# Optimization experiments

Hardware: AMD Instinct MI355X
Metric: run time of the kernel (lower is better)

Reference implementation:

```python
import jax, jax.numpy as jnp
import numpy as np

HEADS = 4
C = 128            # per-head out channels (hard-coded 128 in the module)
NEG_SLOPE_ATT = 0.2   # GATConv attention leaky_relu slope
NEG_SLOPE = 0.01      # F.leaky_relu default slope


def _diag_output_ids(num_groups, n):
    # ids = base_i + n*j + j for group i, agent j; base_i = i * n^2
    i = np.arange(num_groups)[:, None] * (n * n)
    j = np.arange(n)[None, :] * (n + 1)
    return jnp.asarray((i + j).reshape(-1))


def setup_inputs() -> dict:
    key = jax.random.key(0)
    ks = jax.random.split(key, 12)
    num_groups, n_agents = 12, 48
    N = num_groups * n_agents * n_agents      # 27648 nodes
    E = 442368
    F_in, edge_dim, hidden = 256, 16, 256
    s = 0.05
    return {
        "x": jax.random.normal(ks[0], (N, F_in), jnp.float32),
        "edge_index": jax.random.randint(ks[1], (2, E), 0, N, jnp.int32),
        "edge_attr": jax.random.normal(ks[2], (E, edge_dim), jnp.float32),
        "num_groups": num_groups,
        "agents_per_group": n_agents,
        "W": jax.random.normal(ks[3], (F_in, HEADS * C), jnp.float32) * s,
        "att_src": jax.random.normal(ks[4], (HEADS, C), jnp.float32) * s,
        "att_dst": jax.random.normal(ks[5], (HEADS, C), jnp.float32) * s,
        "W_edge": jax.random.normal(ks[6], (edge_dim, HEADS * C), jnp.float32) * s,
        "att_edge": jax.random.normal(ks[7], (HEADS, C), jnp.float32) * s,
        "bias_gat": jnp.zeros((HEADS * C,), jnp.float32),
        "fc_W": jax.random.normal(ks[8], (HEADS * C, hidden), jnp.float32) * s,
        "fc_b": jnp.zeros((hidden,), jnp.float32),
    }


def _gat_conv(x, src, dst, edge_attr_full, W, att_src, att_dst, W_edge, att_edge, bias):
    N = x.shape[0]
    h = (x @ W).reshape(N, HEADS, C)                       # [N,H,C]
    a_src = jnp.einsum('nhc,hc->nh', h, att_src)           # [N,H]
    a_dst = jnp.einsum('nhc,hc->nh', h, att_dst)
    he = (edge_attr_full @ W_edge).reshape(-1, HEADS, C)   # [E',H,C]
    a_edge = jnp.einsum('ehc,hc->eh', he, att_edge)
    logits = jax.nn.leaky_relu(a_src[src] + a_dst[dst] + a_edge, NEG_SLOPE_ATT)
    # segment softmax over incoming edges of each dst node
    m = jax.ops.segment_max(logits, dst, num_segments=N)   # [N,H]
    e = jnp.exp(logits - m[dst])
    s = jax.ops.segment_sum(e, dst, num_segments=N)
    alpha = e / (s[dst] + 1e-16)                           # [E',H]
    msg = h[src] * alpha[..., None]                        # [E',H,C]
    out = jax.ops.segment_sum(msg, dst, num_segments=N)    # [N,H,C]
    return out.reshape(N, HEADS * C) + bias


def reference(x, edge_index, edge_attr, num_groups, agents_per_group,
              W, att_src, att_dst, W_edge, att_edge, bias_gat, fc_W, fc_b):
    N = x.shape[0]
    # add self-loops (PyG default), self-loop edge_attr = mean fill
    loops = jnp.arange(N, dtype=edge_index.dtype)
    src = jnp.concatenate([edge_index[0], loops])
    dst = jnp.concatenate([edge_index[1], loops])
    ea = jnp.concatenate([edge_attr,
                          jnp.broadcast_to(edge_attr.mean(0), (N, edge_attr.shape[1]))])
    h = jax.nn.leaky_relu(
        _gat_conv(x, src, dst, ea, W, att_src, att_dst, W_edge, att_edge, bias_gat),
        NEG_SLOPE)
    ids = _diag_output_ids(num_groups, agents_per_group)
    # fc_output + leaky_relu then diagonal index-select (select first: same math)
    return jax.nn.leaky_relu(h[ids] @ fc_W + fc_b, NEG_SLOPE)
```

## Files before the change

kernel.cpp:

```cpp
#include <hip/hip_runtime.h>

#define NNODES 27648
#define NEDGES 442368
#define FIN    256
#define HC     512
#define NH     4
#define CDIM   128
#define NAG    48
#define NGRP   12
#define N2     2304
#define NOUT   576
#define CAP    128
#define EDIM   16
#define MPART  512
#define SCANB  (NEDGES/256)
#define ASRCB0 (SCANB + 1)


__device__ __forceinline__ float lrelu(float v, float s){ return v > 0.0f ? v : s * v; }

__device__ __forceinline__ float wsum(float v){
  #pragma unroll
  for (int off = 32; off; off >>= 1) v += __shfl_xor(v, off, 64);
  return v;
}
__device__ __forceinline__ float wmax(float v){
  #pragma unroll
  for (int off = 32; off; off >>= 1) v = fmaxf(v, __shfl_xor(v, off, 64));
  return v;
}

__global__ __launch_bounds__(256) void k_pre(
    const float* __restrict__ W, const float* __restrict__ att_src,
    const float* __restrict__ att_dst, const float* __restrict__ W_edge,
    const float* __restrict__ att_edge, const float* __restrict__ ea,
    float* __restrict__ ws_, float* __restrict__ wd_, float* __restrict__ we_,
    int* __restrict__ counts, float4* __restrict__ easum_part){
  int b = blockIdx.x;
  int tid = threadIdx.x;
  if (b < 11) {
    int g = b * 256 + tid;
    if (g < 1024) {
      int f = g >> 2, h = g & 3;
      const float4* wp = (const float4*)(W + f*HC + h*CDIM);
      const float4* ap = (const float4*)(att_src + h*CDIM);
      float s = 0.f;
      #pragma unroll 8
      for (int c4 = 0; c4 < CDIM/4; c4++){
        float4 wv = wp[c4], av = ap[c4];
        s += wv.x*av.x + wv.y*av.y + wv.z*av.z + wv.w*av.w;
      }
      ws_[g] = s;
    } else if (g < 2048) {
      int gg = g - 1024; int f = gg >> 2, h = gg & 3;
      const float4* wp = (const float4*)(W + f*HC + h*CDIM);
      const float4* ap = (const float4*)(att_dst + h*CDIM);
      float s = 0.f;
      #pragma unroll 8
      for (int c4 = 0; c4 < CDIM/4; c4++){
        float4 wv = wp[c4], av = ap[c4];
        s += wv.x*av.x + wv.y*av.y + wv.z*av.z + wv.w*av.w;
      }
      wd_[gg] = s;
    } else if (g < 2112) {
      int gg = g - 2048; int d = gg >> 2, h = gg & 3;
      const float4* wp = (const float4*)(W_edge + d*HC + h*CDIM);
      const float4* ap = (const float4*)(att_edge + h*CDIM);
      float s = 0.f;
      #pragma unroll 8
      for (int c4 = 0; c4 < CDIM/4; c4++){
        float4 wv = wp[c4], av = ap[c4];
        s += wv.x*av.x + wv.y*av.y + wv.z*av.z + wv.w*av.w;
      }
      we_[gg] = s;
    } else if (g < 2112 + NOUT) {
      counts[g - 2112] = 0;
    }
  } else {
    int pb = b - 11;
    const float4* p = (const float4*)ea;
    const int total = NEDGES * 4;
    float4 acc = make_float4(0.f, 0.f, 0.f, 0.f);
    for (int i = pb*256 + tid; i < total; i += MPART*256){
      float4 v = p[i];
      acc.x += v.x; acc.y += v.y; acc.z += v.z; acc.w += v.w;
    }
    #pragma unroll
    for (int off = 4; off <= 32; off <<= 1){
      acc.x += __shfl_xor(acc.x, off, 64);
      acc.y += __shfl_xor(acc.y, off, 64);
      acc.z += __shfl_xor(acc.z, off, 64);
      acc.w += __shfl_xor(acc.w, off, 64);
    }
    __shared__ float4 sd4[16];
    int lane = tid & 63, wave = tid >> 6;
    if (lane < 4) sd4[wave*4 + lane] = acc;
    __syncthreads();
    if (tid < 4){
      float4 t = sd4[tid];
      float4 a = sd4[4+tid], c = sd4[8+tid], d = sd4[12+tid];
      t.x += a.x + c.x + d.x; t.y += a.y + c.y + d.y;
      t.z += a.z + c.z + d.z; t.w += a.w + c.w + d.w;
      easum_part[pb*4 + tid] = t;
    }
  }
}

__global__ __launch_bounds__(256) void k_scan(const int* __restrict__ ei,
    const float* __restrict__ ea, const float* __restrict__ we_,
    const float* __restrict__ ws_, const float* __restrict__ wd_,
    const float* __restrict__ x,
    int* __restrict__ counts, int* __restrict__ slist, float* __restrict__ aed,
    const float* __restrict__ easum_part, float* __restrict__ easum,
    float* __restrict__ mal, float* __restrict__ asrc, float* __restrict__ adst){
  int tid = threadIdx.x;
  int b = blockIdx.x;
  if (b < SCANB){
    int e = b*256 + tid;
    int dst = ei[NEDGES + e];
    int r = dst % N2;
    if (r % 49) return;
    int row = (dst / N2) * NAG + r / 49;
    int pos = atomicAdd(&counts[row], 1);
    if (pos >= CAP) return;
    slist[row*CAP + pos] = ei[e];
    const float* eap = ea + (size_t)e*EDIM;
    float a0=0.f,a1=0.f,a2=0.f,a3=0.f;
    #pragma unroll
    for (int d = 0; d < EDIM; d++){
      float v = eap[d];
      a0 += v*we_[d*4+0]; a1 += v*we_[d*4+1]; a2 += v*we_[d*4+2]; a3 += v*we_[d*4+3];
    }
    float* ap = aed + (size_t)(row*CAP+pos)*4;
    ap[0]=a0; ap[1]=a1; ap[2]=a2; ap[3]=a3;
    return;
  }
  if (b == SCANB){
    int col = tid & 15, part = tid >> 4;
    float s = 0.f;
    for (int pb = 0; pb < MPART/16; pb++)
      s += easum_part[(part*(MPART/16) + pb)*16 + col];
    __shared__ float sd[256];
    __shared__ float se[16];
    sd[tid] = s;
    __syncthreads();
    if (tid < 16){
      float t = 0.f;
      #pragma unroll
      for (int i = 0; i < 16; i++) t += sd[i*16 + tid];
      easum[tid] = t;
      se[tid] = t;
    }
    __syncthreads();
    if (tid < 4){
      const float invE = 1.0f/(float)NEDGES;
      float m = 0.f;
      #pragma unroll
      for (int d = 0; d < 16; d++) m += se[d]*invE*we_[d*4+tid];
      mal[tid] = m;
    }
    return;
  }
  {
    int lane = tid & 63, wave = tid >> 6;
    int node = (b - ASRCB0)*4 + wave;
    float4 xv = *(const float4*)(x + (size_t)node*FIN + lane*4);
    float ps[4] = {0.f,0.f,0.f,0.f}, pd[4] = {0.f,0.f,0.f,0.f};
    #pragma unroll
    for (int q = 0; q < 4; q++){
      float4 wsv = *(const float4*)(ws_ + (lane*4+q)*4);
      float4 wdv = *(const float4*)(wd_ + (lane*4+q)*4);
      float xq = (q==0) ? xv.x : (q==1) ? xv.y : (q==2) ? xv.z : xv.w;
      ps[0]+=xq*wsv.x; ps[1]+=xq*wsv.y; ps[2]+=xq*wsv.z; ps[3]+=xq*wsv.w;
      pd[0]+=xq*wdv.x; pd[1]+=xq*wdv.y; pd[2]+=xq*wdv.z; pd[3]+=xq*wdv.w;
    }
    #pragma unroll
    for (int h = 0; h < 4; h++){ ps[h] = wsum(ps[h]); pd[h] = wsum(pd[h]); }
    if (lane == 0){
      *(float4*)(asrc + (size_t)node*4) = make_float4(ps[0],ps[1],ps[2],ps[3]);
      *(float4*)(adst + (size_t)node*4) = make_float4(pd[0],pd[1],pd[2],pd[3]);
    }
  }
}

__global__ __launch_bounds__(256) void k_attn(const float* __restrict__ x,
    const float* __restrict__ asrc, const float* __restrict__ adst,
    const float* __restrict__ mal,
    const int* __restrict__ counts, const int* __restrict__ slist,
    const float* __restrict__ aed, float* __restrict__ z){
  __shared__ float  lg[(CAP+1)*4];
  __shared__ int    srcs[CAP+1];
  __shared__ float4 pz[4*256];
  int row = blockIdx.x;
  int tid = threadIdx.x;
  int lane = tid & 63, wave = tid >> 6;
  int k = counts[row]; if (k > CAP) k = CAP;
  int g = row / NAG, j = row - g*NAG;
  int dst = g*N2 + j*49;

  if (tid <= k){
    int src; float4 aedv;
    if (tid < k){
      src = slist[row*CAP + tid];
      aedv = *(const float4*)(aed + (size_t)(row*CAP+tid)*4);
    } else {
      src = dst;
      aedv = *(const float4*)mal;
    }
    float4 as = *(const float4*)(asrc + (size_t)src*4);
    float4 ad = *(const float4*)(adst + (size_t)dst*4);
    srcs[tid] = src;
    lg[tid*4+0] = lrelu(as.x + ad.x + aedv.x, 0.2f);
    lg[tid*4+1] = lrelu(as.y + ad.y + aedv.y, 0.2f);
    lg[tid*4+2] = lrelu(as.z + ad.z + aedv.z, 0.2f);
    lg[tid*4+3] = lrelu(as.w + ad.w + aedv.w, 0.2f);
  }
  __syncthreads();

  {
    int h = wave;
    float m = -1e30f;
    for (int i = lane; i <= k; i += 64) m = fmaxf(m, lg[i*4+h]);
    m = wmax(m);
    float s = 0.f;
    for (int i = lane; i <= k; i += 64){
      float e = __expf(lg[i*4+h] - m);
      lg[i*4+h] = e;
      s += e;
    }
    s = wsum(s);
    float inv = 1.0f/(s + 1e-16f);
    for (int i = lane; i <= k; i += 64) lg[i*4+h] *= inv;
  }
  __syncthreads();

  {
    float acc[4][4];
    #pragma unroll
    for (int h = 0; h < 4; h++)
      #pragma unroll
      for (int c = 0; c < 4; c++) acc[h][c] = 0.f;
    for (int i = wave; i <= k; i += 4){
      int src = srcs[i];
      float4 xv = *(const float4*)(x + (size_t)src*FIN + lane*4);
      float a0 = lg[i*4+0], a1 = lg[i*4+1], a2 = lg[i*4+2], a3 = lg[i*4+3];
      acc[0][0] += a0*xv.x; acc[0][1] += a0*xv.y; acc[0][2] += a0*xv.z; acc[0][3] += a0*xv.w;
      acc[1][0] += a1*xv.x; acc[1][1] += a1*xv.y; acc[1][2] += a1*xv.z; acc[1][3] += a1*xv.w;
      acc[2][0] += a2*xv.x; acc[2][1] += a2*xv.y; acc[2][2] += a2*xv.z; acc[2][3] += a2*xv.w;
      acc[3][0] += a3*xv.x; acc[3][1] += a3*xv.y; acc[3][2] += a3*xv.z; acc[3][3] += a3*xv.w;
    }
    #pragma unroll
    for (int h = 0; h < 4; h++)
      pz[wave*256 + h*64 + lane] =
        make_float4(acc[h][0], acc[h][1], acc[h][2], acc[h][3]);
  }
  __syncthreads();
  {
    float4 a = pz[tid], b = pz[256+tid], c = pz[512+tid], d = pz[768+tid];
    ((float4*)(z + (size_t)row*1024))[tid] =
      make_float4(a.x+b.x+c.x+d.x, a.y+b.y+c.y+d.y,
                  a.z+b.z+c.z+d.z, a.w+b.w+c.w+d.w);
  }
}

__global__ __launch_bounds__(256) void k_gemm1(const float* __restrict__ z,
    const float* __restrict__ W, const float* __restrict__ bias,
    float* __restrict__ h2){
  __shared__ float  zt[256][8];
  __shared__ float4 part[8][8][32];
  int rb = blockIdx.x * 8;
  int h  = blockIdx.y;
  int tid = threadIdx.x;
  for (int idx = tid; idx < 2048; idx += 256){
    int r = idx >> 8, f = idx & 255;
    zt[f][r] = z[(size_t)(rb+r)*1024 + h*256 + f];
  }
  __syncthreads();
  {
    int cg = tid & 31, q = tid >> 5;
    const float4* Wp = (const float4*)(W + h*CDIM) + cg;
    float4 acc[8];
    #pragma unroll
    for (int r = 0; r < 8; r++) acc[r] = make_float4(0.f,0.f,0.f,0.f);
    int f0 = q*32;
    #pragma unroll 8
    for (int jf = 0; jf < 32; jf++){
      int f = f0 + jf;
      float4 w4 = Wp[(size_t)f*(HC/4)];
      float4 zlo = *(const float4*)&zt[f][0];
      float4 zhi = *(const float4*)&zt[f][4];
      acc[0].x += zlo.x*w4.x; acc[0].y += zlo.x*w4.y; acc[0].z += zlo.x*w4.z; acc[0].w += zlo.x*w4.w;
      acc[1].x += zlo.y*w4.x; acc[1].y += zlo.y*w4.y; acc[1].z += zlo.y*w4.z; acc[1].w += zlo.y*w4.w;
      acc[2].x += zlo.z*w4.x; acc[2].y += zlo.z*w4.y; acc[2].z += zlo.z*w4.z; acc[2].w += zlo.z*w4.w;
      acc[3].x += zlo.w*w4.x; acc[3].y += zlo.w*w4.y; acc[3].z += zlo.w*w4.z; acc[3].w += zlo.w*w4.w;
      acc[4].x += zhi.x*w4.x; acc[4].y += zhi.x*w4.y; acc[4].z += zhi.x*w4.z; acc[4].w += zhi.x*w4.w;
      acc[5].x += zhi.y*w4.x; acc[5].y += zhi.y*w4.y; acc[5].z += zhi.y*w4.z; acc[5].w += zhi.y*w4.w;
      acc[6].x += zhi.z*w4.x; acc[6].y += zhi.z*w4.y; acc[6].z += zhi.z*w4.z; acc[6].w += zhi.z*w4.w;
      acc[7].x += zhi.w*w4.x; acc[7].y += zhi.w*w4.y; acc[7].z += zhi.w*w4.z; acc[7].w += zhi.w*w4.w;
    }
    #pragma unroll
    for (int r = 0; r < 8; r++) part[q][r][cg] = acc[r];
  }
  __syncthreads();
  {
    int r = tid >> 5, cg = tid & 31;
    float4 s0 = part[0][r][cg];
    #pragma unroll
    for (int q = 1; q < 8; q++){
      float4 t = part[q][r][cg];
      s0.x += t.x; s0.y += t.y; s0.z += t.z; s0.w += t.w;
    }
    float4 bs = ((const float4*)bias)[h*32 + cg];
    float4 o;
    o.x = lrelu(s0.x+bs.x, 0.01f);
    o.y = lrelu(s0.y+bs.y, 0.01f);
    o.z = lrelu(s0.z+bs.z, 0.01f);
    o.w = lrelu(s0.w+bs.w, 0.01f);
    *(float4*)(h2 + (size_t)(rb+r)*HC + h*CDIM + 4*cg) = o;
  }
}

__global__ __launch_bounds__(256) void k_gemm2(const float* __restrict__ h2,
    const float* __restrict__ fcW, const float* __restrict__ fcb,
    float* __restrict__ out){
  __shared__ float  ht[512][8];
  __shared__ float4 part[16][8][16];
  int rb = blockIdx.x * 8;
  int cb = blockIdx.y;
  int tid = threadIdx.x;
  for (int idx = tid; idx < 4096; idx += 256){
    int r = idx >> 9, kf = idx & 511;
    ht[kf][r] = h2[(size_t)(rb+r)*HC + kf];
  }
  __syncthreads();
  {
    int cg = tid & 15, q = tid >> 4;
    const float4* Fp = (const float4*)(fcW + cb*64) + cg;
    float4 acc[8];
    #pragma unroll
    for (int r = 0; r < 8; r++) acc[r] = make_float4(0.f,0.f,0.f,0.f);
    int k0 = q*32;
    #pragma unroll 8
    for (int jk = 0; jk < 32; jk++){
      int kf = k0 + jk;
      float4 w4 = Fp[(size_t)kf*64];
      float4 hlo = *(const float4*)&ht[kf][0];
      float4 hhi = *(const float4*)&ht[kf][4];
      acc[0].x += hlo.x*w4.x; acc[0].y += hlo.x*w4.y; acc[0].z += hlo.x*w4.z; acc[0].w += hlo.x*w4.w;
      acc[1].x += hlo.y*w4.x; acc[1].y += hlo.y*w4.y; acc[1].z += hlo.y*w4.z; acc[1].w += hlo.y*w4.w;
      acc[2].x += hlo.z*w4.x; acc[2].y += hlo.z*w4.y; acc[2].z += hlo.z*w4.z; acc[2].w += hlo.z*w4.w;
      acc[3].x += hlo.w*w4.x; acc[3].y += hlo.w*w4.y; acc[3].z += hlo.w*w4.z; acc[3].w += hlo.w*w4.w;
      acc[4].x += hhi.x*w4.x; acc[4].y += hhi.x*w4.y; acc[4].z += hhi.x*w4.z; acc[4].w += hhi.x*w4.w;
      acc[5].x += hhi.y*w4.x; acc[5].y += hhi.y*w4.y; acc[5].z += hhi.y*w4.z; acc[5].w += hhi.y*w4.w;
      acc[6].x += hhi.z*w4.x; acc[6].y += hhi.z*w4.y; acc[6].z += hhi.z*w4.z; acc[6].w += hhi.z*w4.w;
      acc[7].x += hhi.w*w4.x; acc[7].y += hhi.w*w4.y; acc[7].z += hhi.w*w4.z; acc[7].w += hhi.w*w4.w;
    }
    #pragma unroll
    for (int r = 0; r < 8; r++) part[q][r][cg] = acc[r];
  }
  __syncthreads();
  if (tid < 128){
    int r = tid >> 4, cg = tid & 15;
    float4 s0 = part[0][r][cg];
    #pragma unroll
    for (int q = 1; q < 16; q++){
      float4 t = part[q][r][cg];
      s0.x += t.x; s0.y += t.y; s0.z += t.z; s0.w += t.w;
    }
    float4 bs = ((const float4*)fcb)[cb*16 + cg];
    float4 o;
    o.x = lrelu(s0.x+bs.x, 0.01f);
    o.y = lrelu(s0.y+bs.y, 0.01f);
    o.z = lrelu(s0.z+bs.z, 0.01f);
    o.w = lrelu(s0.w+bs.w, 0.01f);
    *(float4*)(out + (size_t)(rb+r)*256 + cb*64 + 4*cg) = o;
  }
}

extern "C" void kernel_launch(void* const* d_in, const int* in_sizes, int n_in,
                              void* d_out, int out_size, void* d_ws, size_t ws_size,
                              hipStream_t stream) {
  const float* x        = (const float*)d_in[0];
  const int*   ei       = (const int*)  d_in[1];
  const float* ea       = (const float*)d_in[2];
  const float* W        = (const float*)d_in[5];
  const float* att_src  = (const float*)d_in[6];
  const float* att_dst  = (const float*)d_in[7];
  const float* W_edge   = (const float*)d_in[8];
  const float* att_edge = (const float*)d_in[9];
  const float* bias     = (const float*)d_in[10];
  const float* fcW      = (const float*)d_in[11];
  const float* fcb      = (const float*)d_in[12];
  float* out = (float*)d_out;

  float* w = (float*)d_ws;
  float*  ws_       = w;
  float*  wd_       = w + 1024;
  float*  we_       = w + 2048;
  float*  easum     = w + 2112;
  int*    counts    = (int*)(w + 2128);
  float*  easum_p   = w + 2704;
  int*    slist     = (int*)(w + 10896);
  float*  aed       = w + 84624;
  float*  asrc      = w + 379536;
  float*  adst      = w + 490128;
  float*  mal       = w + 600720;
  float*  z         = w + 600724;
  float*  h2        = w + 1190548;

  k_pre<<<11 + MPART, 256, 0, stream>>>(W, att_src, att_dst, W_edge, att_edge, ea,
                                        ws_, wd_, we_, counts, (float4*)easum_p);
  k_scan<<<ASRCB0 + NNODES/4, 256, 0, stream>>>(ei, ea, we_, ws_, wd_, x,
                                                counts, slist, aed,
                                                easum_p, easum, mal, asrc, adst);
  k_attn<<<NOUT, 256, 0, stream>>>(x, asrc, adst, mal, counts, slist, aed, z);
  k_gemm1<<<dim3(NOUT/8, 4), 256, 0, stream>>>(z, W, bias, h2);
  k_gemm2<<<dim3(NOUT/8, 4), 256, 0, stream>>>(h2, fcW, fcb, out);
}
```

Measured before the change: 150.0 us.

## Compute attention scores only for edges into output nodes, fuse binning into pre-pass

Drops the pass that computed source and destination attention scores for all 27648 nodes, which read the whole x matrix. The attention kernel now computes the source and edge scores on the fly, only for the edges binned into each output row, plus the self-loop and destination terms. Edge binning moves into the pre-pass kernel, with counts zeroed by a memset and the edge-attribute mean reduced by float atomics. This removes one kernel launch and most global traffic, at the cost of more per-edge work and gathered x reads inside k_attn.

```diff
diff --git a/kernel.cpp b/kernel.cpp
--- a/kernel.cpp
+++ b/kernel.cpp
@@ -13,8 +13,8 @@
 #define CAP    128
 #define EDIM   16
 #define MPART  512
-#define SCANB  (NEDGES/256)
-#define ASRCB0 (SCANB + 1)
+#define BINB0  (9 + MPART)
+#define PREB   (BINB0 + NEDGES/256)
 
 
 __device__ __forceinline__ float lrelu(float v, float s){ return v > 0.0f ? v : s * v; }
@@ -34,11 +34,12 @@
     const float* __restrict__ W, const float* __restrict__ att_src,
     const float* __restrict__ att_dst, const float* __restrict__ W_edge,
     const float* __restrict__ att_edge, const float* __restrict__ ea,
+    const int* __restrict__ ei,
     float* __restrict__ ws_, float* __restrict__ wd_, float* __restrict__ we_,
-    int* __restrict__ counts, float4* __restrict__ easum_part){
+    float* __restrict__ easum, int* __restrict__ counts, int* __restrict__ slist){
   int b = blockIdx.x;
   int tid = threadIdx.x;
-  if (b < 11) {
+  if (b < 9) {
     int g = b * 256 + tid;
     if (g < 1024) {
       int f = g >> 2, h = g & 3;
@@ -73,11 +74,9 @@
         s += wv.x*av.x + wv.y*av.y + wv.z*av.z + wv.w*av.w;
       }
       we_[gg] = s;
-    } else if (g < 2112 + NOUT) {
-      counts[g - 2112] = 0;
-    }
-  } else {
-    int pb = b - 11;
+    }
+  } else if (b < BINB0) {
+    int pb = b - 9;
     const float4* p = (const float4*)ea;
     const int total = NEDGES * 4;
     float4 acc = make_float4(0.f, 0.f, 0.f, 0.f);
@@ -101,95 +100,32 @@
       float4 a = sd4[4+tid], c = sd4[8+tid], d = sd4[12+tid];
       t.x += a.x + c.x + d.x; t.y += a.y + c.y + d.y;
       t.z += a.z + c.z + d.z; t.w += a.w + c.w + d.w;
-      easum_part[pb*4 + tid] = t;
-    }
-  }
-}
-
-__global__ __launch_bounds__(256) void k_scan(const int* __restrict__ ei,
-    const float* __restrict__ ea, const float* __restrict__ we_,
-    const float* __restrict__ ws_, const float* __restrict__ wd_,
-    const float* __restrict__ x,
-    int* __restrict__ counts, int* __restrict__ slist, float* __restrict__ aed,
-    const float* __restrict__ easum_part, float* __restrict__ easum,
-    float* __restrict__ mal, float* __restrict__ asrc, float* __restrict__ adst){
-  int tid = threadIdx.x;
-  int b = blockIdx.x;
-  if (b < SCANB){
-    int e = b*256 + tid;
+      atomicAdd(&easum[4*tid+0], t.x);
+      atomicAdd(&easum[4*tid+1], t.y);
+      atomicAdd(&easum[4*tid+2], t.z);
+      atomicAdd(&easum[4*tid+3], t.w);
+    }
+  } else {
+    int e = (b - BINB0)*256 + tid;
     int dst = ei[NEDGES + e];
     int r = dst % N2;
     if (r % 49) return;
     int row = (dst / N2) * NAG + r / 49;
     int pos = atomicAdd(&counts[row], 1);
     if (pos >= CAP) return;
-    slist[row*CAP + pos] = ei[e];
-    const float* eap = ea + (size_t)e*EDIM;
-    float a0=0.f,a1=0.f,a2=0.f,a3=0.f;
-    #pragma unroll
-    for (int d = 0; d < EDIM; d++){
-      float v = eap[d];
-      a0 += v*we_[d*4+0]; a1 += v*we_[d*4+1]; a2 += v*we_[d*4+2]; a3 += v*we_[d*4+3];
-    }
-    float* ap = aed + (size_t)(row*CAP+pos)*4;
-    ap[0]=a0; ap[1]=a1; ap[2]=a2; ap[3]=a3;
-    return;
-  }
-  if (b == SCANB){
-    int col = tid & 15, part = tid >> 4;
-    float s = 0.f;
-    for (int pb = 0; pb < MPART/16; pb++)
-      s += easum_part[(part*(MPART/16) + pb)*16 + col];
-    __shared__ float sd[256];
-    __shared__ float se[16];
-    sd[tid] = s;
-    __syncthreads();
-    if (tid < 16){
-      float t = 0.f;
-      #pragma unroll
-      for (int i = 0; i < 16; i++) t += sd[i*16 + tid];
-      easum[tid] = t;
-      se[tid] = t;
-    }
-    __syncthreads();
-    if (tid < 4){
-      const float invE = 1.0f/(float)NEDGES;
-      float m = 0.f;
-      #pragma unroll
-      for (int d = 0; d < 16; d++) m += se[d]*invE*we_[d*4+tid];
-      mal[tid] = m;
-    }
-    return;
-  }
-  {
-    int lane = tid & 63, wave = tid >> 6;
-    int node = (b - ASRCB0)*4 + wave;
-    float4 xv = *(const float4*)(x + (size_t)node*FIN + lane*4);
-    float ps[4] = {0.f,0.f,0.f,0.f}, pd[4] = {0.f,0.f,0.f,0.f};
-    #pragma unroll
-    for (int q = 0; q < 4; q++){
-      float4 wsv = *(const float4*)(ws_ + (lane*4+q)*4);
-      float4 wdv = *(const float4*)(wd_ + (lane*4+q)*4);
-      float xq = (q==0) ? xv.x : (q==1) ? xv.y : (q==2) ? xv.z : xv.w;
-      ps[0]+=xq*wsv.x; ps[1]+=xq*wsv.y; ps[2]+=xq*wsv.z; ps[3]+=xq*wsv.w;
-      pd[0]+=xq*wdv.x; pd[1]+=xq*wdv.y; pd[2]+=xq*wdv.z; pd[3]+=xq*wdv.w;
-    }
-    #pragma unroll
-    for (int h = 0; h < 4; h++){ ps[h] = wsum(ps[h]); pd[h] = wsum(pd[h]); }
-    if (lane == 0){
-      *(float4*)(asrc + (size_t)node*4) = make_float4(ps[0],ps[1],ps[2],ps[3]);
-      *(float4*)(adst + (size_t)node*4) = make_float4(pd[0],pd[1],pd[2],pd[3]);
-    }
+    slist[row*CAP + pos] = e;
   }
 }
 
 __global__ __launch_bounds__(256) void k_attn(const float* __restrict__ x,
-    const float* __restrict__ asrc, const float* __restrict__ adst,
-    const float* __restrict__ mal,
+    const int* __restrict__ ei, const float* __restrict__ ea,
+    const float* __restrict__ ws_, const float* __restrict__ wd_,
+    const float* __restrict__ we_, const float* __restrict__ easum,
     const int* __restrict__ counts, const int* __restrict__ slist,
-    const float* __restrict__ aed, float* __restrict__ z){
+    float* __restrict__ z){
   __shared__ float  lg[(CAP+1)*4];
   __shared__ int    srcs[CAP+1];
+  __shared__ float  adst_s[4];
   __shared__ float4 pz[4*256];
   int row = blockIdx.x;
   int tid = threadIdx.x;
@@ -198,29 +134,72 @@
   int g = row / NAG, j = row - g*NAG;
   int dst = g*N2 + j*49;
 
-  if (tid <= k){
-    int src; float4 aedv;
-    if (tid < k){
-      src = slist[row*CAP + tid];
-      aedv = *(const float4*)(aed + (size_t)(row*CAP+tid)*4);
-    } else {
-      src = dst;
-      aedv = *(const float4*)mal;
-    }
-    float4 as = *(const float4*)(asrc + (size_t)src*4);
-    float4 ad = *(const float4*)(adst + (size_t)dst*4);
-    srcs[tid] = src;
-    lg[tid*4+0] = lrelu(as.x + ad.x + aedv.x, 0.2f);
-    lg[tid*4+1] = lrelu(as.y + ad.y + aedv.y, 0.2f);
-    lg[tid*4+2] = lrelu(as.z + ad.z + aedv.z, 0.2f);
-    lg[tid*4+3] = lrelu(as.w + ad.w + aedv.w, 0.2f);
+  float wsr[4][4];
+  #pragma unroll
+  for (int q = 0; q < 4; q++){
+    float4 t = *(const float4*)(ws_ + (lane*4+q)*4);
+    wsr[q][0]=t.x; wsr[q][1]=t.y; wsr[q][2]=t.z; wsr[q][3]=t.w;
+  }
+  float4 we4 = (lane < 16) ? *(const float4*)(we_ + lane*4)
+                           : make_float4(0.f,0.f,0.f,0.f);
+
+  for (int i = wave; i < k; i += 4){
+    int e = slist[row*CAP + i];
+    int src = ei[e];
+    float eav = (lane < 16) ? ea[(size_t)e*EDIM + lane] : 0.f;
+    float4 xv = *(const float4*)(x + (size_t)src*FIN + lane*4);
+    float p0 = xv.x*wsr[0][0] + xv.y*wsr[1][0] + xv.z*wsr[2][0] + xv.w*wsr[3][0] + eav*we4.x;
+    float p1 = xv.x*wsr[0][1] + xv.y*wsr[1][1] + xv.z*wsr[2][1] + xv.w*wsr[3][1] + eav*we4.y;
+    float p2 = xv.x*wsr[0][2] + xv.y*wsr[1][2] + xv.z*wsr[2][2] + xv.w*wsr[3][2] + eav*we4.z;
+    float p3 = xv.x*wsr[0][3] + xv.y*wsr[1][3] + xv.z*wsr[2][3] + xv.w*wsr[3][3] + eav*we4.w;
+    p0 = wsum(p0); p1 = wsum(p1); p2 = wsum(p2); p3 = wsum(p3);
+    if (lane == 0){
+      srcs[i] = src;
+      lg[i*4+0] = p0; lg[i*4+1] = p1; lg[i*4+2] = p2; lg[i*4+3] = p3;
+    }
+  }
+
+  if (wave == 0){
+    float wdr[4][4];
+    #pragma unroll
+    for (int q = 0; q < 4; q++){
+      float4 t = *(const float4*)(wd_ + (lane*4+q)*4);
+      wdr[q][0]=t.x; wdr[q][1]=t.y; wdr[q][2]=t.z; wdr[q][3]=t.w;
+    }
+    float4 xv = *(const float4*)(x + (size_t)dst*FIN + lane*4);
+    const float invE = 1.0f/(float)NEDGES;
+    float c = (lane < 16) ? easum[lane]*invE : 0.f;
+    float ps[4], pd[4];
+    ps[0] = xv.x*wsr[0][0] + xv.y*wsr[1][0] + xv.z*wsr[2][0] + xv.w*wsr[3][0] + c*we4.x;
+    ps[1] = xv.x*wsr[0][1] + xv.y*wsr[1][1] + xv.z*wsr[2][1] + xv.w*wsr[3][1] + c*we4.y;
+    ps[2] = xv.x*wsr[0][2] + xv.y*wsr[1][2] + xv.z*wsr[2][2] + xv.w*wsr[3][2] + c*we4.z;
+    ps[3] = xv.x*wsr[0][3] + xv.y*wsr[1][3] + xv.z*wsr[2][3] + xv.w*wsr[3][3] + c*we4.w;
+    #pragma unroll
+    for (int h = 0; h < 4; h++){
+      pd[h] = xv.x*wdr[0][h] + xv.y*wdr[1][h] + xv.z*wdr[2][h] + xv.w*wdr[3][h];
+      ps[h] = wsum(ps[h]);
+      pd[h] = wsum(pd[h]);
+    }
+    if (lane == 0){
+      #pragma unroll
+      for (int h = 0; h < 4; h++){
+        adst_s[h] = pd[h];
+        lg[k*4+h] = ps[h];
+      }
+      srcs[k] = dst;
+    }
   }
   __syncthreads();
 
   {
     int h = wave;
+    float ad = adst_s[h];
     float m = -1e30f;
-    for (int i = lane; i <= k; i += 64) m = fmaxf(m, lg[i*4+h]);
+    for (int i = lane; i <= k; i += 64){
+      float v = lrelu(lg[i*4+h] + ad, 0.2f);
+      lg[i*4+h] = v;
+      m = fmaxf(m, v);
+    }
     m = wmax(m);
     float s = 0.f;
     for (int i = lane; i <= k; i += 64){
@@ -399,21 +378,15 @@
   float*  we_       = w + 2048;
   float*  easum     = w + 2112;
   int*    counts    = (int*)(w + 2128);
-  float*  easum_p   = w + 2704;
-  int*    slist     = (int*)(w + 10896);
-  float*  aed       = w + 84624;
-  float*  asrc      = w + 379536;
-  float*  adst      = w + 490128;
-  float*  mal       = w + 600720;
-  float*  z         = w + 600724;
-  float*  h2        = w + 1190548;
-
-  k_pre<<<11 + MPART, 256, 0, stream>>>(W, att_src, att_dst, W_edge, att_edge, ea,
-                                        ws_, wd_, we_, counts, (float4*)easum_p);
-  k_scan<<<ASRCB0 + NNODES/4, 256, 0, stream>>>(ei, ea, we_, ws_, wd_, x,
-                                                counts, slist, aed,
-                                                easum_p, easum, mal, asrc, adst);
-  k_attn<<<NOUT, 256, 0, stream>>>(x, asrc, adst, mal, counts, slist, aed, z);
+  int*    slist     = (int*)(w + 2704);
+  float*  z         = w + 76432;
+  float*  h2        = w + 666256;
+
+  hipMemsetAsync(easum, 0, (16 + NOUT)*sizeof(float), stream);
+  k_pre<<<PREB, 256, 0, stream>>>(W, att_src, att_dst, W_edge, att_edge, ea, ei,
+                                  ws_, wd_, we_, easum, counts, slist);
+  k_attn<<<NOUT, 256, 0, stream>>>(x, ei, ea, ws_, wd_, we_, easum,
+                                   counts, slist, z);
   k_gemm1<<<dim3(NOUT/8, 4), 256, 0, stream>>>(z, W, bias, h2);
   k_gemm2<<<dim3(NOUT/8, 4), 256, 0, stream>>>(h2, fcW, fcb, out);
 }
```

Result: slower. 167.9 us (+11.9%).
